# Optimization experiments

Measured on AMD Instinct MI355X. Metric: run time of the kernel, lower is better.

## Reference

```python
import jax, jax.numpy as jnp
import numpy as np

N_PTS = 65536
N_VERTS = 6890
N_JOINTS = 24


def build_rotation(q):
    # q: [N,4] unnormalized quaternion (r, x, y, z) -> [N,3,3] rotation matrix
    q = q / jnp.linalg.norm(q, axis=-1, keepdims=True)
    r, x, y, z = q[:, 0], q[:, 1], q[:, 2], q[:, 3]
    R = jnp.stack([
        1 - 2 * (y * y + z * z), 2 * (x * y - r * z), 2 * (x * z + r * y),
        2 * (x * y + r * z), 1 - 2 * (x * x + z * z), 2 * (y * z - r * x),
        2 * (x * z - r * y), 2 * (y * z + r * x), 1 - 2 * (x * x + y * y),
    ], axis=-1).reshape(-1, 3, 3)
    return R


def setup_inputs() -> dict:
    key = jax.random.key(0)
    k1, k2, k3, k4, k5 = jax.random.split(key, 5)
    xyz = jax.random.normal(k1, (N_PTS, 3), dtype=jnp.float32)
    rotation = jax.random.normal(k2, (N_PTS, 4), dtype=jnp.float32)
    smpl_verts = jax.random.normal(k3, (N_VERTS, 3), dtype=jnp.float32)
    skinning_weights = jax.random.uniform(k4, (N_VERTS, N_JOINTS), dtype=jnp.float32)
    # row-normalize like real LBS weights
    skinning_weights = skinning_weights / jnp.sum(skinning_weights, axis=-1, keepdims=True)
    bone_transforms = jax.random.normal(k5, (N_JOINTS, 4, 4), dtype=jnp.float32)
    return {"xyz": xyz, "rotation": rotation, "smpl_verts": smpl_verts,
            "skinning_weights": skinning_weights, "bone_transforms": bone_transforms}


def reference(xyz, rotation, smpl_verts, skinning_weights, bone_transforms):
    # --- 1-NN brute-force search (knn_points with K=1) ---
    d2 = (jnp.sum(xyz * xyz, axis=-1, keepdims=True)
          - 2.0 * (xyz @ smpl_verts.T)
          + jnp.sum(smpl_verts * smpl_verts, axis=-1)[None, :])
    p_idx = jnp.argmin(d2, axis=-1)                      # [N]

    # --- skinning-weight gather ---
    pts_W = skinning_weights[p_idx]                      # [N, 24]

    # --- LBS: blend bone transforms ---
    T_fwd = (pts_W @ bone_transforms.reshape(-1, 16)).reshape(-1, 4, 4)  # [N,4,4]

    # --- transform points (homogeneous) ---
    x_bar = jnp.einsum('nij,nj->ni', T_fwd[:, :3, :3], xyz) + T_fwd[:, :3, 3]  # [N,3]

    # --- rotate covariance rotations ---
    rotation_hat = build_rotation(rotation)              # [N,3,3]
    rotation_bar = jnp.einsum('nij,njk->nik', T_fwd[:, :3, :3], rotation_hat)  # [N,3,3]

    return (x_bar, rotation_bar, T_fwd)
```

## Files before the change

kernel.cpp:

```cpp
#include <hip/hip_runtime.h>
#include <math.h>

#define NPTS 65536
#define NV 6890
#define NT 432
#define NTA 440
#define NJ 24
#define NBINS 4096
#define VSPLIT 8
#define WIN 16
#define PTS_PER_BLK 64
#define NBLK (NPTS / PTS_PER_BLK)

typedef double f64x4 __attribute__((ext_vector_type(4)));

__device__ __forceinline__ unsigned mspread(unsigned v) {
    return (v & 1u) | ((v & 2u) << 2) | ((v & 4u) << 4) | ((v & 8u) << 6);
}
__device__ __forceinline__ unsigned morton12(float x, float y, float z) {
    int qx = (int)floorf((x + 4.0f) * 2.0f); qx = qx < 0 ? 0 : (qx > 15 ? 15 : qx);
    int qy = (int)floorf((y + 4.0f) * 2.0f); qy = qy < 0 ? 0 : (qy > 15 ? 15 : qy);
    int qz = (int)floorf((z + 4.0f) * 2.0f); qz = qz < 0 ? 0 : (qz > 15 ? 15 : qz);
    return mspread((unsigned)qx) | (mspread((unsigned)qy) << 1) | (mspread((unsigned)qz) << 2);
}

__global__ void hist2_k(const float* __restrict__ xyz, const float* __restrict__ verts,
                        unsigned* __restrict__ pbins, unsigned* __restrict__ prank,
                        unsigned* __restrict__ vbins, unsigned* __restrict__ vrank) {
    int i = blockIdx.x * blockDim.x + threadIdx.x;
    if (i < NPTS) {
        unsigned c = morton12(xyz[3 * i], xyz[3 * i + 1], xyz[3 * i + 2]);
        prank[i] = atomicAdd(&pbins[c], 1u);
    } else {
        int j = i - NPTS;
        if (j < NV) {
            unsigned c = morton12(verts[3 * j], verts[3 * j + 1], verts[3 * j + 2]);
            vrank[j] = atomicAdd(&vbins[c], 1u);
        }
    }
}

__global__ void prefix_k(const unsigned* __restrict__ pb, const unsigned* __restrict__ vb,
                         unsigned* __restrict__ ps, unsigned* __restrict__ vs) {
    __shared__ unsigned s[NBINS];
    const int tid = threadIdx.x;
    for (int pass = 0; pass < 2; ++pass) {
        const unsigned* in = pass ? vb : pb;
        unsigned* outp = pass ? vs : ps;
        for (int j = tid; j < NBINS; j += 1024) s[j] = in[j];
        __syncthreads();
        for (int off = 1; off < NBINS; off <<= 1) {
            unsigned v[4];
            #pragma unroll
            for (int q = 0; q < 4; ++q) {
                int j = tid + q * 1024;
                v[q] = (j >= off) ? s[j - off] : 0u;
            }
            __syncthreads();
            #pragma unroll
            for (int q = 0; q < 4; ++q) s[tid + q * 1024] += v[q];
            __syncthreads();
        }
        for (int j = tid; j < NBINS; j += 1024) outp[j + 1] = s[j];
        if (tid == 0) outp[0] = 0;
        __syncthreads();
    }
}

__global__ void scatter2_k(const float* __restrict__ xyz, const float* __restrict__ verts,
                           const unsigned* __restrict__ pstart, const unsigned* __restrict__ prank,
                           const unsigned* __restrict__ vstart, const unsigned* __restrict__ vrank,
                           int* __restrict__ pord, int* __restrict__ vord) {
    int i = blockIdx.x * blockDim.x + threadIdx.x;
    if (i < NPTS) {
        unsigned c = morton12(xyz[3 * i], xyz[3 * i + 1], xyz[3 * i + 2]);
        pord[pstart[c] + prank[i]] = i;
    } else {
        int j = i - NPTS;
        if (j < NV) {
            unsigned c = morton12(verts[3 * j], verts[3 * j + 1], verts[3 * j + 2]);
            vord[vstart[c] + vrank[j]] = j;
        }
    }
}

__global__ void prep_frags_k(const float* __restrict__ verts, const int* __restrict__ vord,
                             double* __restrict__ bf, float4* __restrict__ tbb) {
    int e = blockIdx.x * blockDim.x + threadIdx.x;
    if (e < NTA * 64) {
        int l = e & 63;
        int t = e >> 6;
        int pos = t * 16 + (l & 15);
        int k = l >> 4;
        double val;
        if (pos < NV) {
            int j = vord[pos];
            if (k < 3) {
                val = (double)verts[3 * j + k];
            } else {
                double x = (double)verts[3 * j + 0];
                double y = (double)verts[3 * j + 1];
                double z = (double)verts[3 * j + 2];
                val = x * x + y * y + z * z;
            }
        } else {
            val = (k == 3) ? 1e300 : 0.0;
        }
        bf[e] = val;
    }
    if (e < NTA) {
        int t = e;
        if (t * 16 >= NV) { tbb[t] = make_float4(1e30f, 1e30f, 1e30f, 0.0f); return; }
        float mnx = 1e30f, mny = 1e30f, mnz = 1e30f;
        float mxx = -1e30f, mxy = -1e30f, mxz = -1e30f;
        for (int c = 0; c < 16; ++c) {
            int pos = t * 16 + c;
            if (pos >= NV) break;
            int j = vord[pos];
            float x = verts[3 * j], y = verts[3 * j + 1], z = verts[3 * j + 2];
            mnx = fminf(mnx, x); mxx = fmaxf(mxx, x);
            mny = fminf(mny, y); mxy = fmaxf(mxy, y);
            mnz = fminf(mnz, z); mxz = fmaxf(mxz, z);
        }
        float cx = (mnx + mxx) * 0.5f, cy = (mny + mxy) * 0.5f, cz = (mnz + mxz) * 0.5f;
        float r2 = 0.0f;
        for (int c = 0; c < 16; ++c) {
            int pos = t * 16 + c;
            if (pos >= NV) break;
            int j = vord[pos];
            float dx = verts[3 * j] - cx, dy = verts[3 * j + 1] - cy, dz = verts[3 * j + 2] - cz;
            r2 = fmaxf(r2, dx * dx + dy * dy + dz * dz);
        }
        float r = sqrtf(r2) * 1.0002f + 1e-5f;
        tbb[t] = make_float4(cx, cy, cz, r);
    }
}

__device__ __forceinline__ void packmin(double& m, double d, unsigned orv) {
    unsigned long long u = __double_as_longlong(d);
    u = (u & ~0x1FFFULL) | (unsigned long long)orv;
    double t = __longlong_as_double(u);
    asm("v_min_f64 %0, %0, %1" : "+v"(m) : "v"(t));
}

__device__ __forceinline__ void epilogue(int i, int bi,
                                         const float* __restrict__ xyz,
                                         const float* __restrict__ rot,
                                         const float* __restrict__ sw,
                                         const float* __restrict__ bt,
                                         float* __restrict__ out) {
    const float xf = xyz[3 * i + 0];
    const float yf = xyz[3 * i + 1];
    const float zf = xyz[3 * i + 2];

    const float* W = &sw[bi * NJ];
    float Tm[16];
    #pragma unroll
    for (int q = 0; q < 16; ++q) Tm[q] = 0.0f;
    #pragma unroll
    for (int kk = 0; kk < NJ; ++kk) {
        float w = W[kk];
        #pragma unroll
        for (int q = 0; q < 16; ++q) Tm[q] = fmaf(w, bt[16 * kk + q], Tm[q]);
    }

    float xb0 = Tm[0] * xf + Tm[1] * yf + Tm[2]  * zf + Tm[3];
    float xb1 = Tm[4] * xf + Tm[5] * yf + Tm[6]  * zf + Tm[7];
    float xb2 = Tm[8] * xf + Tm[9] * yf + Tm[10] * zf + Tm[11];

    float qr = rot[4 * i + 0];
    float qx = rot[4 * i + 1];
    float qy = rot[4 * i + 2];
    float qz = rot[4 * i + 3];
    float inv = 1.0f / sqrtf(qr * qr + qx * qx + qy * qy + qz * qz);
    qr *= inv; qx *= inv; qy *= inv; qz *= inv;

    float Rh[9];
    Rh[0] = 1.0f - 2.0f * (qy * qy + qz * qz);
    Rh[1] = 2.0f * (qx * qy - qr * qz);
    Rh[2] = 2.0f * (qx * qz + qr * qy);
    Rh[3] = 2.0f * (qx * qy + qr * qz);
    Rh[4] = 1.0f - 2.0f * (qx * qx + qz * qz);
    Rh[5] = 2.0f * (qy * qz - qr * qx);
    Rh[6] = 2.0f * (qx * qz - qr * qy);
    Rh[7] = 2.0f * (qy * qz + qr * qx);
    Rh[8] = 1.0f - 2.0f * (qx * qx + qy * qy);

    float RB[9];
    #pragma unroll
    for (int rr2 = 0; rr2 < 3; ++rr2) {
        #pragma unroll
        for (int cc = 0; cc < 3; ++cc) {
            RB[3 * rr2 + cc] = Tm[4 * rr2 + 0] * Rh[cc]
                             + Tm[4 * rr2 + 1] * Rh[3 + cc]
                             + Tm[4 * rr2 + 2] * Rh[6 + cc];
        }
    }

    out[3 * i + 0] = xb0;
    out[3 * i + 1] = xb1;
    out[3 * i + 2] = xb2;
    float* ob = out + 3 * NPTS + 9 * i;
    #pragma unroll
    for (int q = 0; q < 9; ++q) ob[q] = RB[q];
    float* ot = out + 12 * NPTS + 16 * i;
    #pragma unroll
    for (int q = 0; q < 16; ++q) ot[q] = Tm[q];
}

__launch_bounds__(512)
__global__ void smplnn_scan(const float* __restrict__ xyz,
                            const float* __restrict__ rot,
                            const double* __restrict__ bf,
                            const float* __restrict__ sw,
                            const float* __restrict__ bt,
                            const int* __restrict__ pord,
                            const int* __restrict__ vord,
                            const float4* __restrict__ tbb,
                            const unsigned* __restrict__ vstart,
                            float* __restrict__ out) {
    __shared__ float4 stbb[NTA];
    __shared__ double smin2[VSPLIT][PTS_PER_BLK];
    __shared__ float4 spts[PTS_PER_BLK];
    __shared__ unsigned short slist[448];
    __shared__ int scount;

    const int tid  = threadIdx.x;
    const int lane = tid & 63;
    const int wave = tid >> 6;
    const int r = lane & 15;
    const int k = lane >> 4;
    const int pbase = blockIdx.x * PTS_PER_BLK;

    for (int j = tid; j < NTA; j += 512) stbb[j] = tbb[j];
    if (tid == 0) scount = 0;

    const int o0 = pord[pbase + r];
    const int o1 = pord[pbase + 16 + r];
    const int o2 = pord[pbase + 32 + r];
    const int o3 = pord[pbase + 48 + r];
    double a0 = (k == 3) ? 1.0 : -2.0 * (double)xyz[3 * o0 + k];
    double a1 = (k == 3) ? 1.0 : -2.0 * (double)xyz[3 * o1 + k];
    double a2 = (k == 3) ? 1.0 : -2.0 * (double)xyz[3 * o2 + k];
    double a3 = (k == 3) ? 1.0 : -2.0 * (double)xyz[3 * o3 + k];

    const int om = pord[pbase + lane];
    const float px = xyz[3 * om], py = xyz[3 * om + 1], pz = xyz[3 * om + 2];
    const double pn = (double)px * px + (double)py * py + (double)pz * pz;

    float bxmin = px, bxmax = px, bymin = py, bymax = py, bzmin = pz, bzmax = pz;
    #pragma unroll
    for (int s = 1; s < 64; s <<= 1) {
        bxmin = fminf(bxmin, __shfl_xor(bxmin, s));
        bxmax = fmaxf(bxmax, __shfl_xor(bxmax, s));
        bymin = fminf(bymin, __shfl_xor(bymin, s));
        bymax = fmaxf(bymax, __shfl_xor(bymax, s));
        bzmin = fminf(bzmin, __shfl_xor(bzmin, s));
        bzmax = fmaxf(bzmax, __shfl_xor(bzmax, s));
    }

    const f64x4 zero = {0.0, 0.0, 0.0, 0.0};

    double ar  = (k == 3) ? (double)r : 0.0;
    double one = (k == 3) ? 1.0 : 0.0;
    f64x4 drow = __builtin_amdgcn_mfma_f64_16x16x4f64(ar, one, zero, 0, 0, 0);
    f64x4 dcol = __builtin_amdgcn_mfma_f64_16x16x4f64(one, ar, zero, 0, 0, 0);
    int rowid[4];
    unsigned colb[4];
    #pragma unroll
    for (int v = 0; v < 4; ++v) { rowid[v] = (int)drow[v]; colb[v] = (unsigned)(int)dcol[v]; }

    double m0[4], m1[4], m2[4], m3[4];
    #pragma unroll
    for (int v = 0; v < 4; ++v) { m0[v] = 1e301; m1[v] = 1e301; m2[v] = 1e301; m3[v] = 1e301; }

#define PROCESS(T, B) do {                                                        \
        unsigned tb_ = ((unsigned)(T)) << 4;                                      \
        f64x4 d0 = __builtin_amdgcn_mfma_f64_16x16x4f64(a0, (B), zero, 0, 0, 0);  \
        f64x4 d1 = __builtin_amdgcn_mfma_f64_16x16x4f64(a1, (B), zero, 0, 0, 0);  \
        f64x4 d2 = __builtin_amdgcn_mfma_f64_16x16x4f64(a2, (B), zero, 0, 0, 0);  \
        f64x4 d3 = __builtin_amdgcn_mfma_f64_16x16x4f64(a3, (B), zero, 0, 0, 0);  \
        unsigned q0_ = tb_ | colb[0], q1_ = tb_ | colb[1];                        \
        unsigned q2_ = tb_ | colb[2], q3_ = tb_ | colb[3];                        \
        packmin(m0[0], d0[0], q0_); packmin(m0[1], d0[1], q1_);                   \
        packmin(m0[2], d0[2], q2_); packmin(m0[3], d0[3], q3_);                   \
        packmin(m1[0], d1[0], q0_); packmin(m1[1], d1[1], q1_);                   \
        packmin(m1[2], d1[2], q2_); packmin(m1[3], d1[3], q3_);                   \
        packmin(m2[0], d2[0], q0_); packmin(m2[1], d2[1], q1_);                   \
        packmin(m2[2], d2[2], q2_); packmin(m2[3], d2[3], q3_);                   \
        packmin(m3[0], d3[0], q0_); packmin(m3[1], d3[1], q1_);                   \
        packmin(m3[2], d3[2], q2_); packmin(m3[3], d3[3], q3_);                   \
    } while (0)

    unsigned bc = morton12((bxmin + bxmax) * 0.5f, (bymin + bymax) * 0.5f,
                           (bzmin + bzmax) * 0.5f);
    int tw0 = ((int)vstart[bc] >> 4) - WIN / 2;
    if (tw0 < 0) tw0 = 0;
    if (tw0 > NT - WIN) tw0 = NT - WIN;
    tw0 = __builtin_amdgcn_readfirstlane(tw0);

    {
        int ta = tw0 + 2 * wave;
        double ba = bf[(size_t)ta * 64 + lane];
        double bb2 = bf[(size_t)(ta + 1) * 64 + lane];
        PROCESS(ta, ba);
        PROCESS(ta + 1, bb2);
    }

    auto publish = [&]() {
        double val = 0.0;
        #pragma unroll
        for (int f = 0; f < 4; ++f) {
            #pragma unroll
            for (int v = 0; v < 4; ++v) {
                double q = (f == 0) ? m0[v] : (f == 1) ? m1[v] : (f == 2) ? m2[v] : m3[v];
                #pragma unroll
                for (int s = 1; s < 16; s <<= 1) q = fmin(q, __shfl_xor(q, s, 16));
                if ((lane & 15) == f * 4 + v) val = q;
            }
        }
        smin2[wave][((lane & 15) >> 2) * 16 + rowid[lane & 3]] = val;
    };

    publish();
    __syncthreads();

    double bp_ = smin2[0][lane];
    #pragma unroll
    for (int w = 1; w < VSPLIT; ++w) bp_ = fmin(bp_, smin2[w][lane]);
    double d2p = bp_ + pn;
    if (d2p < 0.0) d2p = 0.0;
    const float sup = sqrtf((float)(d2p * 1.00001 + 1e-8)) + 1e-4f;
    if (wave == 0) spts[lane] = make_float4(px, py, pz, sup);
    __syncthreads();

    if (tid < NT) {
        const int t = tid;
        float4 s0 = stbb[t];
        const float rt = s0.w;
        const float r2t = rt * rt;
        float acc = 1.0f;
        #pragma unroll 4
        for (int p = 0; p < PTS_PER_BLK; ++p) {
            float4 q = spts[p];
            float dx = q.x - s0.x, dy = q.y - s0.y, dz = q.z - s0.z;
            float dist2 = fmaf(dx, dx, fmaf(dy, dy, dz * dz));
            float rhs = fmaf(2.0f * rt, q.w, fmaf(q.w, q.w, r2t));
            acc = fminf(acc, dist2 - rhs);
        }
        bool keep = (acc <= 0.0f) && (t < tw0 || t >= tw0 + WIN);
        if (keep) {
            int p2 = atomicAdd(&scount, 1);
            slist[p2] = (unsigned short)t;
        }
    }
    __syncthreads();

    const int M = scount;
    const int Mp = (M + VSPLIT - 1) & ~(VSPLIT - 1);
    if (tid >= M && tid < Mp) slist[tid] = NT;
    __syncthreads();

    {
        const int nit = Mp / VSPLIT;
        if (nit > 0) {
            int icur = wave;
            int tcur = slist[icur];
            double bcur = bf[(size_t)tcur * 64 + lane];
            for (int j = 0; j < nit; ++j) {
                int inext = icur + VSPLIT;
                int tnext = (j + 1 < nit) ? (int)slist[inext] : NT;
                double bnext = bf[(size_t)tnext * 64 + lane];
                PROCESS(tcur, bcur);
                icur = inext; tcur = tnext; bcur = bnext;
            }
        }
    }

    publish();
    __syncthreads();

    if (wave != 0) return;

    double best = smin2[0][lane];
    #pragma unroll
    for (int w = 1; w < VSPLIT; ++w) best = fmin(best, smin2[w][lane]);
    const int bpos = (int)(__double_as_longlong(best) & 0x1FFFULL);
    const int bi = vord[bpos];
    const int oi = pord[pbase + lane];
    epilogue(oi, bi, xyz, rot, sw, bt, out);
#undef PROCESS
}

extern "C" void kernel_launch(void* const* d_in, const int* in_sizes, int n_in,
                              void* d_out, int out_size, void* d_ws, size_t ws_size,
                              hipStream_t stream) {
    const float* xyz   = (const float*)d_in[0];
    const float* rot   = (const float*)d_in[1];
    const float* verts = (const float*)d_in[2];
    const float* sw    = (const float*)d_in[3];
    const float* bt    = (const float*)d_in[4];
    float* out = (float*)d_out;

    double*   bfrag  = (double*)d_ws;
    float4*   tbb    = (float4*)(bfrag + NTA * 64);
    int*      pord   = (int*)(tbb + NTA);
    int*      vord   = pord + NPTS;
    unsigned* prank  = (unsigned*)(vord + 6912);
    unsigned* vrank  = prank + NPTS;
    unsigned* pbins  = vrank + 6912;
    unsigned* vbins  = pbins + NBINS;
    unsigned* pstart = vbins + NBINS;
    unsigned* vstart = pstart + NBINS + 4;

    hipMemsetAsync(pbins, 0, 2 * NBINS * sizeof(unsigned), stream);

    hist2_k<<<(NPTS + NV + 255) / 256, 256, 0, stream>>>(xyz, verts, pbins, prank, vbins, vrank);
    prefix_k<<<1, 1024, 0, stream>>>(pbins, vbins, pstart, vstart);
    scatter2_k<<<(NPTS + NV + 255) / 256, 256, 0, stream>>>(xyz, verts, pstart, prank,
                                                            vstart, vrank, pord, vord);
    prep_frags_k<<<(NTA * 64 + 255) / 256, 256, 0, stream>>>(verts, vord, bfrag, tbb);

    smplnn_scan<<<NBLK, 512, 0, stream>>>(xyz, rot, bfrag, sw, bt,
                                          pord, vord, tbb, vstart, out);
}
```

Before: 119.1 us.

## Use wave-level shuffle scan for prefix sums and per-wave seed tile windows

The prefix-sum kernel swaps its shared-memory Hillis-Steele scan, which needed many barriers, for a register-based per-thread plus wave-shuffle scan that handles both histograms in one pass. The NN scan no longer computes a block bounding box and one 16-tile seed window. Each wave instead picks its own pair of seed tiles from the Morton cell of one of its points, offset by wave index, and publishes it to shared memory so the pruning pass can exclude those tiles. The aim is tighter initial bounds and fewer shuffles, at the risk of seed windows that overlap or bound less well.

```diff
diff --git a/kernel.cpp b/kernel.cpp
--- a/kernel.cpp
+++ b/kernel.cpp
@@ -8,7 +8,6 @@
 #define NJ 24
 #define NBINS 4096
 #define VSPLIT 8
-#define WIN 16
 #define PTS_PER_BLK 64
 #define NBLK (NPTS / PTS_PER_BLK)
 
@@ -42,29 +41,47 @@
 
 __global__ void prefix_k(const unsigned* __restrict__ pb, const unsigned* __restrict__ vb,
                          unsigned* __restrict__ ps, unsigned* __restrict__ vs) {
-    __shared__ unsigned s[NBINS];
+    __shared__ unsigned wsumA[16], wsumB[16];
     const int tid = threadIdx.x;
-    for (int pass = 0; pass < 2; ++pass) {
-        const unsigned* in = pass ? vb : pb;
-        unsigned* outp = pass ? vs : ps;
-        for (int j = tid; j < NBINS; j += 1024) s[j] = in[j];
-        __syncthreads();
-        for (int off = 1; off < NBINS; off <<= 1) {
-            unsigned v[4];
-            #pragma unroll
-            for (int q = 0; q < 4; ++q) {
-                int j = tid + q * 1024;
-                v[q] = (j >= off) ? s[j - off] : 0u;
-            }
-            __syncthreads();
-            #pragma unroll
-            for (int q = 0; q < 4; ++q) s[tid + q * 1024] += v[q];
-            __syncthreads();
-        }
-        for (int j = tid; j < NBINS; j += 1024) outp[j + 1] = s[j];
-        if (tid == 0) outp[0] = 0;
-        __syncthreads();
-    }
+    const int lane = tid & 63, wave = tid >> 6;
+    const int base = tid * 4;
+    unsigned a0 = pb[base], a1 = pb[base + 1], a2 = pb[base + 2], a3 = pb[base + 3];
+    unsigned b0 = vb[base], b1 = vb[base + 1], b2 = vb[base + 2], b3 = vb[base + 3];
+    unsigned ia0 = a0, ia1 = ia0 + a1, ia2 = ia1 + a2, ia3 = ia2 + a3;
+    unsigned ib0 = b0, ib1 = ib0 + b1, ib2 = ib1 + b2, ib3 = ib2 + b3;
+    unsigned ta = ia3, tb = ib3;
+    #pragma unroll
+    for (int d = 1; d < 64; d <<= 1) {
+        unsigned va = __shfl_up(ta, d);
+        unsigned vb2 = __shfl_up(tb, d);
+        if (lane >= d) { ta += va; tb += vb2; }
+    }
+    if (lane == 63) { wsumA[wave] = ta; wsumB[wave] = tb; }
+    __syncthreads();
+    if (wave == 0 && lane < 16) {
+        unsigned sa = wsumA[lane], sb = wsumB[lane];
+        #pragma unroll
+        for (int d = 1; d < 16; d <<= 1) {
+            unsigned va = __shfl_up(sa, d, 16);
+            unsigned vb2 = __shfl_up(sb, d, 16);
+            if ((lane & 15) >= d) { sa += va; sb += vb2; }
+        }
+        wsumA[lane] = sa; wsumB[lane] = sb;
+    }
+    __syncthreads();
+    const unsigned waveOffA = (wave > 0) ? wsumA[wave - 1] : 0u;
+    const unsigned waveOffB = (wave > 0) ? wsumB[wave - 1] : 0u;
+    const unsigned thrExclA = waveOffA + (ta - ia3);
+    const unsigned thrExclB = waveOffB + (tb - ib3);
+    ps[base + 1] = thrExclA + ia0;
+    ps[base + 2] = thrExclA + ia1;
+    ps[base + 3] = thrExclA + ia2;
+    ps[base + 4] = thrExclA + ia3;
+    vs[base + 1] = thrExclB + ib0;
+    vs[base + 2] = thrExclB + ib1;
+    vs[base + 3] = thrExclB + ib2;
+    vs[base + 4] = thrExclB + ib3;
+    if (tid == 0) { ps[0] = 0; vs[0] = 0; }
 }
 
 __global__ void scatter2_k(const float* __restrict__ xyz, const float* __restrict__ verts,
@@ -222,6 +239,7 @@
     __shared__ float4 stbb[NTA];
     __shared__ double smin2[VSPLIT][PTS_PER_BLK];
     __shared__ float4 spts[PTS_PER_BLK];
+    __shared__ int swin[VSPLIT];
     __shared__ unsigned short slist[448];
     __shared__ int scount;
 
@@ -248,16 +266,13 @@
     const float px = xyz[3 * om], py = xyz[3 * om + 1], pz = xyz[3 * om + 2];
     const double pn = (double)px * px + (double)py * py + (double)pz * pz;
 
-    float bxmin = px, bxmax = px, bymin = py, bymax = py, bzmin = pz, bzmax = pz;
-    #pragma unroll
-    for (int s = 1; s < 64; s <<= 1) {
-        bxmin = fminf(bxmin, __shfl_xor(bxmin, s));
-        bxmax = fmaxf(bxmax, __shfl_xor(bxmax, s));
-        bymin = fminf(bymin, __shfl_xor(bymin, s));
-        bymax = fmaxf(bymax, __shfl_xor(bymax, s));
-        bzmin = fminf(bzmin, __shfl_xor(bzmin, s));
-        bzmax = fmaxf(bzmax, __shfl_xor(bzmax, s));
-    }
+    const unsigned mycell = morton12(px, py, pz);
+    const unsigned cw = (unsigned)__shfl((int)mycell, 8 * wave + 4);
+    int tw = ((int)vstart[cw] >> 4) + 2 * wave - 7;
+    if (tw < 0) tw = 0;
+    if (tw > NT - 2) tw = NT - 2;
+    tw = __builtin_amdgcn_readfirstlane(tw);
+    if (lane == 0) swin[wave] = tw;
 
     const f64x4 zero = {0.0, 0.0, 0.0, 0.0};
 
@@ -292,19 +307,11 @@
         packmin(m3[2], d3[2], q2_); packmin(m3[3], d3[3], q3_);                   \
     } while (0)
 
-    unsigned bc = morton12((bxmin + bxmax) * 0.5f, (bymin + bymax) * 0.5f,
-                           (bzmin + bzmax) * 0.5f);
-    int tw0 = ((int)vstart[bc] >> 4) - WIN / 2;
-    if (tw0 < 0) tw0 = 0;
-    if (tw0 > NT - WIN) tw0 = NT - WIN;
-    tw0 = __builtin_amdgcn_readfirstlane(tw0);
-
     {
-        int ta = tw0 + 2 * wave;
-        double ba = bf[(size_t)ta * 64 + lane];
-        double bb2 = bf[(size_t)(ta + 1) * 64 + lane];
-        PROCESS(ta, ba);
-        PROCESS(ta + 1, bb2);
+        double ba = bf[(size_t)tw * 64 + lane];
+        double bb2 = bf[(size_t)(tw + 1) * 64 + lane];
+        PROCESS(tw, ba);
+        PROCESS(tw + 1, bb2);
     }
 
     auto publish = [&]() {
@@ -348,7 +355,13 @@
             float rhs = fmaf(2.0f * rt, q.w, fmaf(q.w, q.w, r2t));
             acc = fminf(acc, dist2 - rhs);
         }
-        bool keep = (acc <= 0.0f) && (t < tw0 || t >= tw0 + WIN);
+        bool excl = false;
+        #pragma unroll
+        for (int w = 0; w < VSPLIT; ++w) {
+            int tw_ = swin[w];
+            excl = excl || (t >= tw_ && t < tw_ + 2);
+        }
+        bool keep = (acc <= 0.0f) && !excl;
         if (keep) {
             int p2 = atomicAdd(&scount, 1);
             slist[p2] = (unsigned short)t;
```

New measurement: 120.1 us. Within noise of the previous version (+0.8%).

## Fuse preprocessing kernels into one cooperative kernel with grid syncs

Applied to the files above, without the earlier changes.

Replaces the memset plus four preprocessing kernels (histogram, prefix, scatter, fragment prep) with a single cooperative kernel of 128x1024 threads, separated by grid-wide syncs. The bin prefix scan is rewritten as a wave-shuffle scan in block 0, replacing the shared-memory Hillis-Steele loop with its many barriers. The aim is to remove per-launch overhead and inter-kernel gaps for these small stages. In exchange it adds the cost of four grid barriers, and everything depends on cooperative launch residency.

```diff
diff --git a/kernel.cpp b/kernel.cpp
--- a/kernel.cpp
+++ b/kernel.cpp
@@ -1,5 +1,8 @@
 #include <hip/hip_runtime.h>
+#include <hip/hip_cooperative_groups.h>
 #include <math.h>
+
+namespace cg = cooperative_groups;
 
 #define NPTS 65536
 #define NV 6890
@@ -24,72 +27,90 @@
     return mspread((unsigned)qx) | (mspread((unsigned)qy) << 1) | (mspread((unsigned)qz) << 2);
 }
 
-__global__ void hist2_k(const float* __restrict__ xyz, const float* __restrict__ verts,
-                        unsigned* __restrict__ pbins, unsigned* __restrict__ prank,
-                        unsigned* __restrict__ vbins, unsigned* __restrict__ vrank) {
-    int i = blockIdx.x * blockDim.x + threadIdx.x;
-    if (i < NPTS) {
-        unsigned c = morton12(xyz[3 * i], xyz[3 * i + 1], xyz[3 * i + 2]);
-        prank[i] = atomicAdd(&pbins[c], 1u);
+__global__ void prep_all_k(const float* __restrict__ xyz, const float* __restrict__ verts,
+                           unsigned* __restrict__ pbins, unsigned* __restrict__ prank,
+                           unsigned* __restrict__ vbins, unsigned* __restrict__ vrank,
+                           unsigned* __restrict__ pstart, unsigned* __restrict__ vstart,
+                           int* __restrict__ pord, int* __restrict__ vord,
+                           double* __restrict__ bf, float4* __restrict__ tbb) {
+    cg::grid_group grid = cg::this_grid();
+    __shared__ unsigned wsumA[16], wsumB[16];
+    const int gtid = blockIdx.x * blockDim.x + threadIdx.x;
+
+    if (gtid < 2 * NBINS) pbins[gtid] = 0;
+    grid.sync();
+
+    if (gtid < NPTS) {
+        unsigned c = morton12(xyz[3 * gtid], xyz[3 * gtid + 1], xyz[3 * gtid + 2]);
+        prank[gtid] = atomicAdd(&pbins[c], 1u);
     } else {
-        int j = i - NPTS;
+        int j = gtid - NPTS;
         if (j < NV) {
             unsigned c = morton12(verts[3 * j], verts[3 * j + 1], verts[3 * j + 2]);
             vrank[j] = atomicAdd(&vbins[c], 1u);
         }
     }
-}
-
-__global__ void prefix_k(const unsigned* __restrict__ pb, const unsigned* __restrict__ vb,
-                         unsigned* __restrict__ ps, unsigned* __restrict__ vs) {
-    __shared__ unsigned s[NBINS];
-    const int tid = threadIdx.x;
-    for (int pass = 0; pass < 2; ++pass) {
-        const unsigned* in = pass ? vb : pb;
-        unsigned* outp = pass ? vs : ps;
-        for (int j = tid; j < NBINS; j += 1024) s[j] = in[j];
+    grid.sync();
+
+    if (blockIdx.x == 0) {
+        const int tid = threadIdx.x;
+        const int lane = tid & 63, wave = tid >> 6;
+        const int base = tid * 4;
+        unsigned a0 = pbins[base], a1 = pbins[base + 1], a2 = pbins[base + 2], a3 = pbins[base + 3];
+        unsigned b0 = vbins[base], b1 = vbins[base + 1], b2 = vbins[base + 2], b3 = vbins[base + 3];
+        unsigned ia0 = a0, ia1 = ia0 + a1, ia2 = ia1 + a2, ia3 = ia2 + a3;
+        unsigned ib0 = b0, ib1 = ib0 + b1, ib2 = ib1 + b2, ib3 = ib2 + b3;
+        unsigned ta = ia3, tb = ib3;
+        #pragma unroll
+        for (int d = 1; d < 64; d <<= 1) {
+            unsigned va = __shfl_up(ta, d);
+            unsigned vb2 = __shfl_up(tb, d);
+            if (lane >= d) { ta += va; tb += vb2; }
+        }
+        if (lane == 63) { wsumA[wave] = ta; wsumB[wave] = tb; }
         __syncthreads();
-        for (int off = 1; off < NBINS; off <<= 1) {
-            unsigned v[4];
+        if (wave == 0 && lane < 16) {
+            unsigned sa = wsumA[lane], sb = wsumB[lane];
             #pragma unroll
-            for (int q = 0; q < 4; ++q) {
-                int j = tid + q * 1024;
-                v[q] = (j >= off) ? s[j - off] : 0u;
-            }
-            __syncthreads();
-            #pragma unroll
-            for (int q = 0; q < 4; ++q) s[tid + q * 1024] += v[q];
-            __syncthreads();
-        }
-        for (int j = tid; j < NBINS; j += 1024) outp[j + 1] = s[j];
-        if (tid == 0) outp[0] = 0;
+            for (int d = 1; d < 16; d <<= 1) {
+                unsigned va = __shfl_up(sa, d, 16);
+                unsigned vb2 = __shfl_up(sb, d, 16);
+                if ((lane & 15) >= d) { sa += va; sb += vb2; }
+            }
+            wsumA[lane] = sa; wsumB[lane] = sb;
+        }
         __syncthreads();
-    }
-}
-
-__global__ void scatter2_k(const float* __restrict__ xyz, const float* __restrict__ verts,
-                           const unsigned* __restrict__ pstart, const unsigned* __restrict__ prank,
-                           const unsigned* __restrict__ vstart, const unsigned* __restrict__ vrank,
-                           int* __restrict__ pord, int* __restrict__ vord) {
-    int i = blockIdx.x * blockDim.x + threadIdx.x;
-    if (i < NPTS) {
-        unsigned c = morton12(xyz[3 * i], xyz[3 * i + 1], xyz[3 * i + 2]);
-        pord[pstart[c] + prank[i]] = i;
+        const unsigned waveOffA = (wave > 0) ? wsumA[wave - 1] : 0u;
+        const unsigned waveOffB = (wave > 0) ? wsumB[wave - 1] : 0u;
+        const unsigned thrExclA = waveOffA + (ta - ia3);
+        const unsigned thrExclB = waveOffB + (tb - ib3);
+        pstart[base + 1] = thrExclA + ia0;
+        pstart[base + 2] = thrExclA + ia1;
+        pstart[base + 3] = thrExclA + ia2;
+        pstart[base + 4] = thrExclA + ia3;
+        vstart[base + 1] = thrExclB + ib0;
+        vstart[base + 2] = thrExclB + ib1;
+        vstart[base + 3] = thrExclB + ib2;
+        vstart[base + 4] = thrExclB + ib3;
+        if (tid == 0) { pstart[0] = 0; vstart[0] = 0; }
+    }
+    grid.sync();
+
+    if (gtid < NPTS) {
+        unsigned c = morton12(xyz[3 * gtid], xyz[3 * gtid + 1], xyz[3 * gtid + 2]);
+        pord[pstart[c] + prank[gtid]] = gtid;
     } else {
-        int j = i - NPTS;
+        int j = gtid - NPTS;
         if (j < NV) {
             unsigned c = morton12(verts[3 * j], verts[3 * j + 1], verts[3 * j + 2]);
             vord[vstart[c] + vrank[j]] = j;
         }
     }
-}
-
-__global__ void prep_frags_k(const float* __restrict__ verts, const int* __restrict__ vord,
-                             double* __restrict__ bf, float4* __restrict__ tbb) {
-    int e = blockIdx.x * blockDim.x + threadIdx.x;
-    if (e < NTA * 64) {
-        int l = e & 63;
-        int t = e >> 6;
+    grid.sync();
+
+    if (gtid < NTA * 64) {
+        int l = gtid & 63;
+        int t = gtid >> 6;
         int pos = t * 16 + (l & 15);
         int k = l >> 4;
         double val;
@@ -106,33 +127,36 @@
         } else {
             val = (k == 3) ? 1e300 : 0.0;
         }
-        bf[e] = val;
-    }
-    if (e < NTA) {
-        int t = e;
-        if (t * 16 >= NV) { tbb[t] = make_float4(1e30f, 1e30f, 1e30f, 0.0f); return; }
-        float mnx = 1e30f, mny = 1e30f, mnz = 1e30f;
-        float mxx = -1e30f, mxy = -1e30f, mxz = -1e30f;
-        for (int c = 0; c < 16; ++c) {
-            int pos = t * 16 + c;
-            if (pos >= NV) break;
-            int j = vord[pos];
-            float x = verts[3 * j], y = verts[3 * j + 1], z = verts[3 * j + 2];
-            mnx = fminf(mnx, x); mxx = fmaxf(mxx, x);
-            mny = fminf(mny, y); mxy = fmaxf(mxy, y);
-            mnz = fminf(mnz, z); mxz = fmaxf(mxz, z);
-        }
-        float cx = (mnx + mxx) * 0.5f, cy = (mny + mxy) * 0.5f, cz = (mnz + mxz) * 0.5f;
-        float r2 = 0.0f;
-        for (int c = 0; c < 16; ++c) {
-            int pos = t * 16 + c;
-            if (pos >= NV) break;
-            int j = vord[pos];
-            float dx = verts[3 * j] - cx, dy = verts[3 * j + 1] - cy, dz = verts[3 * j + 2] - cz;
-            r2 = fmaxf(r2, dx * dx + dy * dy + dz * dz);
-        }
-        float r = sqrtf(r2) * 1.0002f + 1e-5f;
-        tbb[t] = make_float4(cx, cy, cz, r);
+        bf[gtid] = val;
+    }
+    if (gtid < NTA) {
+        int t = gtid;
+        if (t * 16 >= NV) {
+            tbb[t] = make_float4(1e30f, 1e30f, 1e30f, 0.0f);
+        } else {
+            float mnx = 1e30f, mny = 1e30f, mnz = 1e30f;
+            float mxx = -1e30f, mxy = -1e30f, mxz = -1e30f;
+            for (int c = 0; c < 16; ++c) {
+                int pos = t * 16 + c;
+                if (pos >= NV) break;
+                int j = vord[pos];
+                float x = verts[3 * j], y = verts[3 * j + 1], z = verts[3 * j + 2];
+                mnx = fminf(mnx, x); mxx = fmaxf(mxx, x);
+                mny = fminf(mny, y); mxy = fmaxf(mxy, y);
+                mnz = fminf(mnz, z); mxz = fmaxf(mxz, z);
+            }
+            float cx = (mnx + mxx) * 0.5f, cy = (mny + mxy) * 0.5f, cz = (mnz + mxz) * 0.5f;
+            float r2 = 0.0f;
+            for (int c = 0; c < 16; ++c) {
+                int pos = t * 16 + c;
+                if (pos >= NV) break;
+                int j = vord[pos];
+                float dx = verts[3 * j] - cx, dy = verts[3 * j + 1] - cy, dz = verts[3 * j + 2] - cz;
+                r2 = fmaxf(r2, dx * dx + dy * dy + dz * dz);
+            }
+            float r = sqrtf(r2) * 1.0002f + 1e-5f;
+            tbb[t] = make_float4(cx, cy, cz, r);
+        }
     }
 }
 
@@ -413,13 +437,11 @@
     unsigned* pstart = vbins + NBINS;
     unsigned* vstart = pstart + NBINS + 4;
 
-    hipMemsetAsync(pbins, 0, 2 * NBINS * sizeof(unsigned), stream);
-
-    hist2_k<<<(NPTS + NV + 255) / 256, 256, 0, stream>>>(xyz, verts, pbins, prank, vbins, vrank);
-    prefix_k<<<1, 1024, 0, stream>>>(pbins, vbins, pstart, vstart);
-    scatter2_k<<<(NPTS + NV + 255) / 256, 256, 0, stream>>>(xyz, verts, pstart, prank,
-                                                            vstart, vrank, pord, vord);
-    prep_frags_k<<<(NTA * 64 + 255) / 256, 256, 0, stream>>>(verts, vord, bfrag, tbb);
+    void* args[] = { (void*)&xyz, (void*)&verts,
+                     (void*)&pbins, (void*)&prank, (void*)&vbins, (void*)&vrank,
+                     (void*)&pstart, (void*)&vstart, (void*)&pord, (void*)&vord,
+                     (void*)&bfrag, (void*)&tbb };
+    hipLaunchCooperativeKernel((void*)prep_all_k, dim3(128), dim3(1024), args, 0, stream);
 
     smplnn_scan<<<NBLK, 512, 0, stream>>>(xyz, rot, bfrag, sw, bt,
                                           pord, vord, tbb, vstart, out);
```

Measured after the change: 169.7 us. 42.4% more time.
